# Performance work log

Measured on AMD Instinct MI355X. Metric: run time of the kernel, lower is better.

Reference implementation:

```python
import jax, jax.numpy as jnp
import numpy as np

B, S, D = 8, 8192, 64
N_HASHES = 8
BUCKET_SIZE = 64
N_BUCKETS = S // BUCKET_SIZE  # 128
SELF_ATTN_VALUE = -5e4  # torch reformer TOKEN_SELF_ATTN_VALUE


def setup_inputs() -> dict:
    key = jax.random.key(0)
    k1, k2, k3 = jax.random.split(key, 3)
    qk = jax.random.normal(k1, (B, S, D), dtype=jnp.float32)
    v = jax.random.normal(k2, (B, S, D), dtype=jnp.float32)
    # LSH random rotations: (dim, n_hashes, n_buckets // 2), shared across batch/heads
    rotations = jax.random.normal(k3, (D, N_HASHES, N_BUCKETS // 2), dtype=jnp.float32)
    return {"qk": qk, "v": v, "rotations": rotations, "query_len": S}


def _look_one_back(x):
    # concatenate each chunk with the preceding chunk (wrapping) along the kv axis
    x_extra = jnp.concatenate([x[:, -1:], x[:, :-1]], axis=1)
    return jnp.concatenate([x, x_extra], axis=2)


def _lsh_bucketed_dots(qk, v, rotations):
    batch, seqlen, dim = qk.shape
    n_buckets = seqlen // BUCKET_SIZE
    # --- hash vectors: rotate, concat with negation, argmax -> bucket ids ---
    rotated = jnp.einsum('btf,fhi->bhti', qk, rotations)           # (B, H, S, nb/2)
    rotated = jnp.concatenate([rotated, -rotated], axis=-1)        # (B, H, S, nb)
    buckets = jnp.argmax(rotated, axis=-1)                         # (B, H, S) int
    offsets = (jnp.arange(N_HASHES) * n_buckets)[None, :, None]    # disjoint per round
    buckets = (buckets + offsets).reshape(batch, -1)               # (B, H*S)

    # --- stable bucket sort via composite key (all keys unique) ---
    ticker = jnp.arange(N_HASHES * seqlen)[None, :]                # (1, H*S)
    buckets_and_t = seqlen * buckets + (ticker % seqlen)
    sticker = jnp.argsort(buckets_and_t, axis=-1)                  # sort permutation
    undo_sort = jnp.argsort(sticker, axis=-1)                      # inverse permutation
    st = sticker % seqlen                                          # original token ids

    # --- gather tokens into bucket order ---
    sqk = jnp.take_along_axis(qk, st[..., None], axis=1)           # (B, H*S, D)
    sv = jnp.take_along_axis(v, st[..., None], axis=1)

    n_chunks = N_HASHES * n_buckets
    bq_t = st.reshape(batch, n_chunks, BUCKET_SIZE)                # (B, C, bs)
    bqk = sqk.reshape(batch, n_chunks, BUCKET_SIZE, dim)
    bv = sv.reshape(batch, n_chunks, BUCKET_SIZE, dim)

    bq = bqk
    bk = bqk / (jnp.linalg.norm(bqk, axis=-1, keepdims=True) + 1e-6)  # unit-length keys

    bk = _look_one_back(bk)       # (B, C, 2*bs, D)
    bv = _look_one_back(bv)
    bkv_t = _look_one_back(bq_t)  # (B, C, 2*bs)

    dots = jnp.einsum('buie,buje->buij', bq, bk) * (dim ** -0.5)   # (B, C, bs, 2*bs)
    self_mask = bq_t[:, :, :, None] == bkv_t[:, :, None, :]
    dots = jnp.where(self_mask, SELF_ATTN_VALUE, dots)
    return dots, undo_sort, bv


def reference(qk, v, rotations, query_len):
    batch, seqlen, dim = qk.shape
    dots, undo_sort, bv = _lsh_bucketed_dots(qk, v, rotations)
    dots_logsumexp = jax.nn.logsumexp(dots, axis=-1, keepdims=True)
    p = jnp.exp(dots - dots_logsumexp)                             # per-bucket softmax
    bo = jnp.einsum('buij,buje->buie', p, bv)                      # (B, C, bs, D)
    so = bo.reshape(batch, -1, dim)                                # (B, H*S, D)
    slogits = dots_logsumexp.reshape(batch, -1)                    # (B, H*S)
    # undo the bucket sort
    o = jnp.take_along_axis(so, undo_sort[..., None], axis=1)
    logits = jnp.take_along_axis(slogits, undo_sort, axis=1)
    o = o.reshape(batch, N_HASHES, seqlen, dim)[:, :, :query_len]
    logits = logits.reshape(batch, N_HASHES, seqlen, 1)[:, :, :query_len]
    # combine across hash rounds, weighted by per-round logsumexp
    probs = jnp.exp(logits - jax.nn.logsumexp(logits, axis=1, keepdims=True))
    out = jnp.sum(o * probs, axis=1)                               # (B, query_len, D)
    return out
```

## Files before the change

### kernel.cpp

```cpp
#include <hip/hip_runtime.h>
#include <math.h>

#define B_  8
#define S_  8192
#define D_  64
#define H_  8
#define NB_ 128
#define NC_ 1024
#define REP_CAP 65536
#define T2_ 2e-3f

typedef _Float16 f16x8 __attribute__((ext_vector_type(8)));
typedef _Float16 f16x2 __attribute__((ext_vector_type(2)));
typedef float    f32x4 __attribute__((ext_vector_type(4)));
typedef unsigned int uint_;

#define MFMA16(A, Bv, C) __builtin_amdgcn_mfma_f32_16x16x32_f16(A, Bv, C, 0, 0, 0)

__global__ __launch_bounds__(256) void prep_rot_kernel(
    const float* __restrict__ rot, _Float16* __restrict__ rotHi,
    _Float16* __restrict__ rotLo, int* __restrict__ cnt)
{
  __shared__ float rs[64 * 64];
  const int tid = threadIdx.x, h = blockIdx.x;
  if (h == 0 && tid == 0) *cnt = 0;
#pragma unroll
  for (int it = 0; it < 16; ++it) {
    const int f = it * 4 + (tid >> 6), i = tid & 63;
    rs[f * 64 + i] = rot[f * 512 + h * 64 + i];
  }
  __syncthreads();
  const int i = tid & 63, grp = tid >> 6;
  _Float16 hi[16], lo[16];
#pragma unroll
  for (int ff = 0; ff < 16; ++ff) {
    const float x = rs[(grp * 16 + ff) * 64 + i];
    hi[ff] = (_Float16)x;
    lo[ff] = (_Float16)(x - (float)hi[ff]);
  }
  f16x8* dH = (f16x8*)(rotHi + h * 4096 + i * 64 + grp * 16);
  f16x8* dL = (f16x8*)(rotLo + h * 4096 + i * 64 + grp * 16);
  dH[0] = ((f16x8*)hi)[0]; dH[1] = ((f16x8*)hi)[1];
  dL[0] = ((f16x8*)lo)[0]; dL[1] = ((f16x8*)lo)[1];
}

__global__ __launch_bounds__(256) void prep_tok_kernel(
    const float* __restrict__ qk, const float* __restrict__ v,
    _Float16* __restrict__ q16, _Float16* __restrict__ kn16,
    _Float16* __restrict__ v16)
{
  const int gt = blockIdx.x * 64 + (threadIdx.x >> 2);
  const int qu = threadIdx.x & 3;
  const size_t off = (size_t)gt * 64 + qu * 16;
  float x[16];
#pragma unroll
  for (int k = 0; k < 4; ++k) ((float4*)x)[k] = ((const float4*)(qk + off))[k];
  float ss = 0.f;
#pragma unroll
  for (int k = 0; k < 16; ++k) ss = fmaf(x[k], x[k], ss);
  ss += __shfl_xor(ss, 1); ss += __shfl_xor(ss, 2);
  const float inv = 0.125f / (sqrtf(ss) + 1e-6f);
  f16x8 qh[2], kn[2];
#pragma unroll
  for (int j = 0; j < 16; ++j) {
    qh[j >> 3][j & 7] = (_Float16)x[j];
    kn[j >> 3][j & 7] = (_Float16)(x[j] * inv);
  }
  ((f16x8*)(q16  + off))[0] = qh[0]; ((f16x8*)(q16  + off))[1] = qh[1];
  ((f16x8*)(kn16 + off))[0] = kn[0]; ((f16x8*)(kn16 + off))[1] = kn[1];
  float y[16];
#pragma unroll
  for (int k = 0; k < 4; ++k) ((float4*)y)[k] = ((const float4*)(v + off))[k];
  f16x8 vv[2];
#pragma unroll
  for (int j = 0; j < 16; ++j) vv[j >> 3][j & 7] = (_Float16)y[j];
  ((f16x8*)(v16 + off))[0] = vv[0]; ((f16x8*)(v16 + off))[1] = vv[1];
}

__global__ __launch_bounds__(256) void hash_kernel(
    const float* __restrict__ qk,
    const _Float16* __restrict__ rotHi, const _Float16* __restrict__ rotLo,
    int* __restrict__ bucket, int* __restrict__ cnt, int2* __restrict__ list)
{
  __shared__ _Float16 rH[64 * 72];
  __shared__ _Float16 rL[64 * 72];
  const int tid  = threadIdx.x;
  const int tile = blockIdx.x & 127;
  const int b    = blockIdx.x >> 7;
  const int lane = tid & 63, w = tid >> 6;
  const int m16  = lane & 15, qd = lane >> 4;

  const int t = tile * 64 + w * 16 + m16;
  f16x8 BH0, BH1, BL0, BL1;
  {
    const float* src = qk + ((size_t)b * S_ + t) * 64 + 8 * qd;
    float x[16];
    ((float4*)x)[0] = ((const float4*)src)[0];
    ((float4*)x)[1] = ((const float4*)(src + 4))[0];
    ((float4*)x)[2] = ((const float4*)(src + 32))[0];
    ((float4*)x)[3] = ((const float4*)(src + 36))[0];
#pragma unroll
    for (int j = 0; j < 8; ++j) {
      const _Float16 h0 = (_Float16)x[j];
      BH0[j] = h0; BL0[j] = (_Float16)(x[j] - (float)h0);
      const _Float16 h1 = (_Float16)x[j + 8];
      BH1[j] = h1; BL1[j] = (_Float16)(x[j + 8] - (float)h1);
    }
  }
  const int srow = tid >> 2, scol = (tid & 3) * 16;
  const uint_ qd16 = (uint_)(qd << 4);

#pragma unroll 1
  for (int h = 0; h < 8; ++h) {
    __syncthreads();
    {
      const _Float16* sH = rotHi + h * 4096 + srow * 64 + scol;
      const _Float16* sL = rotLo + h * 4096 + srow * 64 + scol;
      *(f16x8*)(rH + srow * 72 + scol)     = ((const f16x8*)sH)[0];
      *(f16x8*)(rH + srow * 72 + scol + 8) = ((const f16x8*)sH)[1];
      *(f16x8*)(rL + srow * 72 + scol)     = ((const f16x8*)sL)[0];
      *(f16x8*)(rL + srow * 72 + scol + 8) = ((const f16x8*)sL)[1];
    }
    __syncthreads();

    f32x4 acc[4];
#pragma unroll
    for (int mt = 0; mt < 4; ++mt) acc[mt] = (f32x4){0.f, 0.f, 0.f, 0.f};
#pragma unroll
    for (int mt = 0; mt < 4; ++mt) {
      const _Float16* aH = rH + (16 * mt + m16) * 72 + 8 * qd;
      const _Float16* aL = rL + (16 * mt + m16) * 72 + 8 * qd;
      const f16x8 AH0 = *(const f16x8*)aH;
      const f16x8 AH1 = *(const f16x8*)(aH + 32);
      const f16x8 AL0 = *(const f16x8*)aL;
      const f16x8 AL1 = *(const f16x8*)(aL + 32);
      acc[mt] = MFMA16(AH0, BH0, acc[mt]);
      acc[mt] = MFMA16(AH1, BH1, acc[mt]);
      acc[mt] = MFMA16(AH0, BL0, acc[mt]);
      acc[mt] = MFMA16(AH1, BL1, acc[mt]);
      acc[mt] = MFMA16(AL0, BH0, acc[mt]);
      acc[mt] = MFMA16(AL1, BH1, acc[mt]);
    }

    float v1M = -1e30f, v2M = -1e30f, v1m = 1e30f, v2m = 1e30f;
#pragma unroll
    for (int mt = 0; mt < 4; ++mt)
#pragma unroll
      for (int rg = 0; rg < 4; ++rg) {
        uint_ u = __float_as_uint(acc[mt][rg]);
        u = (u & 0xFFFFFFC0u) | qd16 | (uint_)((mt << 2) | rg);
        const float xk = __uint_as_float(u);
        v2M = __builtin_amdgcn_fmed3f(v1M, v2M, xk);
        v1M = fmaxf(v1M, xk);
        v2m = __builtin_amdgcn_fmed3f(v1m, v2m, xk);
        v1m = fminf(v1m, xk);
      }
#pragma unroll
    for (int off = 16; off <= 32; off <<= 1) {
      const float o1M = __shfl_xor(v1M, off), o2M = __shfl_xor(v2M, off);
      v2M = __builtin_amdgcn_fmed3f(v1M, o1M, fmaxf(v2M, o2M));
      v1M = fmaxf(v1M, o1M);
      const float o1m = __shfl_xor(v1m, off), o2m = __shfl_xor(v2m, off);
      v2m = __builtin_amdgcn_fmed3f(v1m, o1m, fminf(v2m, o2m));
      v1m = fminf(v1m, o1m);
    }
    if (qd == 0) {
      const uint_ cM = __float_as_uint(v1M) & 63u;
      const uint_ cm = __float_as_uint(v1m) & 63u;
      const int ixM = 16 * (int)((cM >> 2) & 3u) + 4 * (int)(cM >> 4) + (int)(cM & 3u);
      const int ixm = 16 * (int)((cm >> 2) & 3u) + 4 * (int)(cm >> 4) + (int)(cm & 3u);
      const int bkt = (v1M >= -v1m) ? ixM : 64 + ixm;
      bucket[((size_t)(b * 8 + h)) * S_ + t] = bkt;
      const bool flag = ((v1M - v2M) < T2_) | ((v2m - v1m) < T2_) |
                        (fabsf(v1M + v1m) < T2_);
      if (flag) {
        const int s = atomicAdd(cnt, 1);
        if (s < REP_CAP) list[s] = make_int2(b * 8 + h, t);
      }
    }
  }
}

__global__ __launch_bounds__(256) void repair_kernel(
    const float* __restrict__ qk, const float* __restrict__ rot,
    const int* __restrict__ cnt, const int2* __restrict__ list,
    int* __restrict__ bucket)
{
  const int n = min(*cnt, REP_CAP);
  const int lane = threadIdx.x & 63;
  const int wid  = (blockIdx.x * 256 + threadIdx.x) >> 6;
  const int nw   = gridDim.x * 4;
  for (int idx = wid; idx < n; idx += nw) {
    const int bh = list[idx].x, t = list[idx].y;
    const int b = bh >> 3, hh = bh & 7;
    const float* qrow = qk + ((size_t)b * S_ + t) * D_;
    const float* rcol = rot + hh * 64 + lane;
    double acc = 0.0;
#pragma unroll 8
    for (int f = 0; f < 64; ++f)
      acc = fma((double)qrow[f], (double)rcol[(size_t)f * 512], acc);
    double vM = acc; int iM = lane;
    double vm = acc; int im = lane;
#pragma unroll
    for (int off = 32; off >= 1; off >>= 1) {
      const double voM = __shfl_xor(vM, off); const int ioM = __shfl_xor(iM, off);
      if (voM > vM || (voM == vM && ioM < iM)) { vM = voM; iM = ioM; }
      const double vom = __shfl_xor(vm, off); const int iom = __shfl_xor(im, off);
      if (vom < vm || (vom == vm && iom < im)) { vm = vom; im = iom; }
    }
    if (lane == 0) {
      const int bkt = (vM >= -vm) ? iM : 64 + im;
      bucket[(size_t)bh * S_ + t] = bkt;
    }
  }
}

__global__ __launch_bounds__(1024) void sort_kernel(
    const int* __restrict__ bucket, int* __restrict__ st)
{
  __shared__ uint_ hist[64 * 128];
  __shared__ unsigned short lb[S_];
  __shared__ int off[128];
  const int tid = threadIdx.x;
  const int bh  = blockIdx.x;
  const size_t base = (size_t)bh * S_;

#pragma unroll
  for (int k = 0; k < 8; ++k) hist[tid + k * 1024] = 0;
  __syncthreads();

#pragma unroll
  for (int k = 0; k < 8; ++k) {
    const int t = k * 1024 + tid;
    const int bk = bucket[base + t];
    lb[t] = (unsigned short)bk;
    const int g = t >> 6;
    atomicAdd(&hist[(g & 63) * 128 + bk], 1u << (16 * (g >> 6)));
  }
  __syncthreads();

  if (tid < 128) {
    uint_ s = 0;
#pragma unroll
    for (int g = 0; g < 64; ++g) {
      const uint_ wv = hist[g * 128 + tid];
      s += (wv & 0xFFFFu) + (wv >> 16);
    }
    off[tid] = (int)s;
  }
  __syncthreads();
  if (tid == 0) {
    int run = 0;
    for (int k = 0; k < 128; ++k) { const int c = off[k]; off[k] = run; run += c; }
  }
  __syncthreads();
  if (tid < 128) {
    uint_ run = (uint_)off[tid];
#pragma unroll
    for (int g = 0; g < 64; ++g) {
      const uint_ wv = hist[g * 128 + tid];
      hist[g * 128 + tid] = (wv & 0xFFFF0000u) | run;
      run += (wv & 0xFFFFu);
    }
#pragma unroll
    for (int g = 0; g < 64; ++g) {
      const uint_ wv = hist[g * 128 + tid];
      hist[g * 128 + tid] = (wv & 0xFFFFu) | (run << 16);
      run += (wv >> 16);
    }
  }
  __syncthreads();

  const int lane = tid & 63, wv_ = tid >> 6;
  const int b = bh >> 3, h = bh & 7;
  const size_t stb = (size_t)b * (H_ * S_) + (size_t)h * S_;
  const unsigned long long ltmask = (1ull << lane) - 1ull;
#pragma unroll
  for (int k = 0; k < 8; ++k) {
    const int g = wv_ * 8 + k;
    const int t = g * 64 + lane;
    const int bk = (int)lb[t];
    unsigned long long same = ~0ull;
#pragma unroll
    for (int bit = 0; bit < 7; ++bit) {
      const unsigned long long m = __ballot((bk >> bit) & 1);
      same &= ((bk >> bit) & 1) ? m : ~m;
    }
    const int rloc = __popcll(same & ltmask);
    const uint_ wd = hist[(g & 63) * 128 + bk];
    const int gbase = (int)((wd >> (16 * (g >> 6))) & 0xFFFFu);
    st[stb + gbase + rloc] = t;
  }
}

__global__ __launch_bounds__(256, 8) void attn_kernel(
    const _Float16* __restrict__ q16, const _Float16* __restrict__ kn16,
    const _Float16* __restrict__ v16, const int* __restrict__ st,
    _Float16* __restrict__ so, float* __restrict__ slog)
{
  __shared__ _Float16 smem[64 * 136];
  __shared__ __align__(16) int sIds[128];

  const int tid = threadIdx.x;
  const int c   = blockIdx.x & (NC_ - 1);
  const int b   = blockIdx.x >> 10;
  const int cm1 = (c + NC_ - 1) & (NC_ - 1);
  const size_t bst = (size_t)b * (H_ * S_);
  const size_t row0 = bst + (size_t)c * 64;
  const size_t row1 = bst + (size_t)cm1 * 64;

  const int lane = tid & 63;
  const int w    = tid >> 6;
  const int m16  = lane & 15;
  const int qd   = lane >> 4;

  if (tid < 128) sIds[tid] = (tid < 64) ? st[row0 + tid] : st[row1 + tid - 64];

  const int rid = st[row0 + 16 * w + m16];
  f16x8 q0, q1;
  {
    const _Float16* qp = q16 + ((size_t)b * S_ + rid) * 64 + 8 * qd;
    q0 = *(const f16x8*)qp;
    q1 = *(const f16x8*)(qp + 32);
  }

  const int r = tid >> 2, qu = tid & 3;
  {
    const int tok = st[row0 + r];
    const f16x8* sk = (const f16x8*)(kn16 + ((size_t)b * S_ + tok) * 64 + qu * 16);
    *(f16x8*)(smem + r * 72 + qu * 16)     = sk[0];
    *(f16x8*)(smem + r * 72 + qu * 16 + 8) = sk[1];
  }
  __syncthreads();

  f32x4 acc[8];
#pragma unroll
  for (int jt = 0; jt < 8; ++jt) acc[jt] = (f32x4){0.f, 0.f, 0.f, 0.f};

#pragma unroll
  for (int jt = 0; jt < 4; ++jt) {
    const _Float16* krow = smem + (16 * jt + m16) * 72;
    const f16x8 kb0 = *(const f16x8*)(krow + 8 * qd);
    const f16x8 kb1 = *(const f16x8*)(krow + 32 + 8 * qd);
    acc[jt] = MFMA16(kb0, q0, acc[jt]);
    acc[jt] = MFMA16(kb1, q1, acc[jt]);
  }
  __syncthreads();

  {
    const int tok = sIds[64 + r];
    const f16x8* sk = (const f16x8*)(kn16 + ((size_t)b * S_ + tok) * 64 + qu * 16);
    *(f16x8*)(smem + r * 72 + qu * 16)     = sk[0];
    *(f16x8*)(smem + r * 72 + qu * 16 + 8) = sk[1];
  }
  __syncthreads();

#pragma unroll
  for (int jt = 4; jt < 8; ++jt) {
    const _Float16* krow = smem + (16 * (jt - 4) + m16) * 72;
    const f16x8 kb0 = *(const f16x8*)(krow + 8 * qd);
    const f16x8 kb1 = *(const f16x8*)(krow + 32 + 8 * qd);
    acc[jt] = MFMA16(kb0, q0, acc[jt]);
    acc[jt] = MFMA16(kb1, q1, acc[jt]);
  }

  float m = -1e30f;
#pragma unroll
  for (int jt = 0; jt < 8; ++jt) {
    const int4 cid = *(const int4*)(sIds + 16 * jt + 4 * qd);
    float x;
    x = acc[jt][0]; if (cid.x == rid) x = -5e4f; acc[jt][0] = x; m = fmaxf(m, x);
    x = acc[jt][1]; if (cid.y == rid) x = -5e4f; acc[jt][1] = x; m = fmaxf(m, x);
    x = acc[jt][2]; if (cid.z == rid) x = -5e4f; acc[jt][2] = x; m = fmaxf(m, x);
    x = acc[jt][3]; if (cid.w == rid) x = -5e4f; acc[jt][3] = x; m = fmaxf(m, x);
  }
  m = fmaxf(m, __shfl_xor(m, 16));
  m = fmaxf(m, __shfl_xor(m, 32));
  float sum = 0.f;
#pragma unroll
  for (int jt = 0; jt < 8; ++jt)
#pragma unroll
    for (int rg = 0; rg < 4; ++rg) {
      const float e = __expf(acc[jt][rg] - m);
      acc[jt][rg] = e;
      sum += e;
    }
  sum += __shfl_xor(sum, 16);
  sum += __shfl_xor(sum, 32);
  const float rinv = 1.f / sum;

  const int hh = c >> 7;
  const size_t hb = ((size_t)(b * 8 + hh)) * S_;
  if (qd == 0) slog[hb + rid] = m + __logf(sum);

  f16x8 pa[4];
#pragma unroll
  for (int s = 0; s < 4; ++s)
#pragma unroll
    for (int j = 0; j < 8; ++j)
      pa[s][j] = (_Float16)acc[2 * s + (j >> 2)][j & 3];

  const int jp = r;
  const int c0 = 2 * jp;
  const int k0 = 32 * (c0 >> 5) + 16 * ((c0 >> 2) & 1) + 4 * ((c0 >> 3) & 3) + (c0 & 3);
  const int tok0 = sIds[k0], tok1 = sIds[k0 + 1];
  f16x8 va[2], vb[2];
  {
    const f16x8* s0 = (const f16x8*)(v16 + ((size_t)b * S_ + tok0) * 64 + qu * 16);
    const f16x8* s1 = (const f16x8*)(v16 + ((size_t)b * S_ + tok1) * 64 + qu * 16);
    va[0] = s0[0]; va[1] = s0[1];
    vb[0] = s1[0]; vb[1] = s1[1];
  }
  __syncthreads();

  {
    const int swz = (qu << 3) ^ ((qu & 1) << 5);
    _Float16* dst = smem + (c0 ^ swz);
#pragma unroll
    for (int jj = 0; jj < 16; ++jj) {
      const int d = 16 * qu + jj;
      f16x2 pk; pk[0] = va[jj >> 3][jj & 7]; pk[1] = vb[jj >> 3][jj & 7];
      *(f16x2*)(dst + d * 136) = pk;
    }
  }
  __syncthreads();

  f32x4 oacc[4];
#pragma unroll
  for (int dt = 0; dt < 4; ++dt) oacc[dt] = (f32x4){0.f, 0.f, 0.f, 0.f};
#pragma unroll
  for (int s = 0; s < 4; ++s) {
#pragma unroll
    for (int dt = 0; dt < 4; ++dt) {
      const _Float16* vp = smem + (16 * dt + m16) * 136
                         + 32 * (s ^ (dt & 1)) + 8 * (qd ^ dt);
      const f16x8 bv = *(const f16x8*)vp;
      oacc[dt] = MFMA16(pa[s], bv, oacc[dt]);
    }
  }

  const int4 rid4 = *(const int4*)(sIds + 16 * w + 4 * qd);
  const int ridv[4] = {rid4.x, rid4.y, rid4.z, rid4.w};
  float rin[4];
#pragma unroll
  for (int rg = 0; rg < 4; ++rg) rin[rg] = __shfl(rinv, 4 * qd + rg);
#pragma unroll
  for (int dt = 0; dt < 4; ++dt)
#pragma unroll
    for (int rg = 0; rg < 4; ++rg)
      so[(hb + ridv[rg]) * 64 + 16 * dt + m16] = (_Float16)(oacc[dt][rg] * rin[rg]);
}

__global__ __launch_bounds__(256) void combine_kernel(
    const _Float16* __restrict__ so, const float* __restrict__ slog,
    float* __restrict__ out)
{
  const int gt = blockIdx.x * 4 + (threadIdx.x >> 6);
  const int d  = threadIdx.x & 63;
  const int b  = gt >> 13;
  const int t  = gt & (S_ - 1);

  float l[8];
#pragma unroll
  for (int h = 0; h < 8; ++h)
    l[h] = slog[((size_t)(b * 8 + h)) * S_ + t];
  float m = l[0];
#pragma unroll
  for (int h = 1; h < 8; ++h) m = fmaxf(m, l[h]);
  float wv[8], W = 0.f;
#pragma unroll
  for (int h = 0; h < 8; ++h) { wv[h] = expf(l[h] - m); W += wv[h]; }
  const float iW = 1.f / W;
  float acc = 0.f;
#pragma unroll
  for (int h = 0; h < 8; ++h)
    acc = fmaf(wv[h], (float)so[(((size_t)(b * 8 + h)) * S_ + t) * 64 + d], acc);
  out[(size_t)gt * 64 + d] = acc * iW;
}

extern "C" void kernel_launch(void* const* d_in, const int* in_sizes, int n_in,
                              void* d_out, int out_size, void* d_ws, size_t ws_size,
                              hipStream_t stream)
{
  const float* qk  = (const float*)d_in[0];
  const float* v   = (const float*)d_in[1];
  const float* rot = (const float*)d_in[2];
  float* out = (float*)d_out;

  char* ws = (char*)d_ws;
  const size_t MB = 1ull << 20, KB = 1024;
  int*      bucket = (int*)      (ws + 0 * MB);
  int*      st     = (int*)      (ws + 2 * MB);
  float*    slog   = (float*)    (ws + 4 * MB);
  _Float16* q16    = (_Float16*) (ws + 8 * MB);
  _Float16* kn16   = (_Float16*) (ws + 16 * MB);
  _Float16* v16    = (_Float16*) (ws + 24 * MB);
  _Float16* rotHi  = (_Float16*) (ws + 32 * MB);
  _Float16* rotLo  = (_Float16*) (ws + 32 * MB + 64 * KB);
  int*      cnt    = (int*)      (ws + 32 * MB + 128 * KB);
  int2*     list   = (int2*)     (ws + 32 * MB + 192 * KB);
  _Float16* so     = (_Float16*) (ws + 33 * MB);
  if (ws_size < 98 * MB) return;

  hipLaunchKernelGGL(prep_rot_kernel, dim3(8),           dim3(256),  0, stream, rot, rotHi, rotLo, cnt);
  hipLaunchKernelGGL(prep_tok_kernel, dim3(1024),        dim3(256),  0, stream, qk, v, q16, kn16, v16);
  hipLaunchKernelGGL(hash_kernel,     dim3(8 * 128),     dim3(256),  0, stream, qk, rotHi, rotLo, bucket, cnt, list);
  hipLaunchKernelGGL(repair_kernel,   dim3(128),         dim3(256),  0, stream, qk, rot, cnt, list, bucket);
  hipLaunchKernelGGL(sort_kernel,     dim3(64),          dim3(1024), 0, stream, bucket, st);
  hipLaunchKernelGGL(attn_kernel,     dim3(B_ * NC_),    dim3(256),  0, stream, q16, kn16, v16, st, so, slog);
  hipLaunchKernelGGL(combine_kernel,  dim3(B_ * S_ / 4), dim3(256),  0, stream, so, slog, out);
}
```

Baseline: 195.0 us.

## Merge prep kernels, stage attention output through LDS, vectorize combine

Folds the rotation-prep and token-prep kernels into one launch, with the first 8 blocks handling the rotations. The attention kernel now writes its normalized output tile to shared memory and then stores each token row as 16-byte vectors, replacing scattered 2-byte global stores. The combine kernel gives each thread 8 output dims and uses vectorized f16x8 loads and float4 stores. Together these aim to cut launch overhead and uncoalesced memory traffic, at the cost of extra barriers in the attention kernel.

```diff
diff --git a/kernel.cpp b/kernel.cpp
--- a/kernel.cpp
+++ b/kernel.cpp
@@ -17,40 +17,42 @@
 
 #define MFMA16(A, Bv, C) __builtin_amdgcn_mfma_f32_16x16x32_f16(A, Bv, C, 0, 0, 0)
 
-__global__ __launch_bounds__(256) void prep_rot_kernel(
+__global__ __launch_bounds__(256) void prep_kernel(
     const float* __restrict__ rot, _Float16* __restrict__ rotHi,
-    _Float16* __restrict__ rotLo, int* __restrict__ cnt)
-{
-  __shared__ float rs[64 * 64];
-  const int tid = threadIdx.x, h = blockIdx.x;
-  if (h == 0 && tid == 0) *cnt = 0;
-#pragma unroll
-  for (int it = 0; it < 16; ++it) {
-    const int f = it * 4 + (tid >> 6), i = tid & 63;
-    rs[f * 64 + i] = rot[f * 512 + h * 64 + i];
-  }
-  __syncthreads();
-  const int i = tid & 63, grp = tid >> 6;
-  _Float16 hi[16], lo[16];
-#pragma unroll
-  for (int ff = 0; ff < 16; ++ff) {
-    const float x = rs[(grp * 16 + ff) * 64 + i];
-    hi[ff] = (_Float16)x;
-    lo[ff] = (_Float16)(x - (float)hi[ff]);
-  }
-  f16x8* dH = (f16x8*)(rotHi + h * 4096 + i * 64 + grp * 16);
-  f16x8* dL = (f16x8*)(rotLo + h * 4096 + i * 64 + grp * 16);
-  dH[0] = ((f16x8*)hi)[0]; dH[1] = ((f16x8*)hi)[1];
-  dL[0] = ((f16x8*)lo)[0]; dL[1] = ((f16x8*)lo)[1];
-}
-
-__global__ __launch_bounds__(256) void prep_tok_kernel(
+    _Float16* __restrict__ rotLo, int* __restrict__ cnt,
     const float* __restrict__ qk, const float* __restrict__ v,
     _Float16* __restrict__ q16, _Float16* __restrict__ kn16,
     _Float16* __restrict__ v16)
 {
-  const int gt = blockIdx.x * 64 + (threadIdx.x >> 2);
-  const int qu = threadIdx.x & 3;
+  __shared__ float rs[64 * 64];
+  const int tid = threadIdx.x;
+
+  if (blockIdx.x < 8) {
+    const int h = blockIdx.x;
+    if (h == 0 && tid == 0) *cnt = 0;
+#pragma unroll
+    for (int it = 0; it < 16; ++it) {
+      const int f = it * 4 + (tid >> 6), i = tid & 63;
+      rs[f * 64 + i] = rot[f * 512 + h * 64 + i];
+    }
+    __syncthreads();
+    const int i = tid & 63, grp = tid >> 6;
+    _Float16 hi[16], lo[16];
+#pragma unroll
+    for (int ff = 0; ff < 16; ++ff) {
+      const float x = rs[(grp * 16 + ff) * 64 + i];
+      hi[ff] = (_Float16)x;
+      lo[ff] = (_Float16)(x - (float)hi[ff]);
+    }
+    f16x8* dH = (f16x8*)(rotHi + h * 4096 + i * 64 + grp * 16);
+    f16x8* dL = (f16x8*)(rotLo + h * 4096 + i * 64 + grp * 16);
+    dH[0] = ((f16x8*)hi)[0]; dH[1] = ((f16x8*)hi)[1];
+    dL[0] = ((f16x8*)lo)[0]; dL[1] = ((f16x8*)lo)[1];
+    return;
+  }
+
+  const int gt = (blockIdx.x - 8) * 64 + (tid >> 2);
+  const int qu = tid & 3;
   const size_t off = (size_t)gt * 64 + qu * 16;
   float x[16];
 #pragma unroll
@@ -400,8 +402,7 @@
     for (int j = 0; j < 8; ++j)
       pa[s][j] = (_Float16)acc[2 * s + (j >> 2)][j & 3];
 
-  const int jp = r;
-  const int c0 = 2 * jp;
+  const int c0 = 2 * r;
   const int k0 = 32 * (c0 >> 5) + 16 * ((c0 >> 2) & 1) + 4 * ((c0 >> 3) & 3) + (c0 & 3);
   const int tok0 = sIds[k0], tok1 = sIds[k0 + 1];
   f16x8 va[2], vb[2];
@@ -434,36 +435,47 @@
     for (int dt = 0; dt < 4; ++dt) {
       const _Float16* vp = smem + (16 * dt + m16) * 136
                          + 32 * (s ^ (dt & 1)) + 8 * (qd ^ dt);
-      const f16x8 bv = *(const f16x8*)vp;
+      const f16x8 bv = *(const f16x8*)(vp);
       oacc[dt] = MFMA16(pa[s], bv, oacc[dt]);
     }
   }
 
-  const int4 rid4 = *(const int4*)(sIds + 16 * w + 4 * qd);
-  const int ridv[4] = {rid4.x, rid4.y, rid4.z, rid4.w};
   float rin[4];
 #pragma unroll
   for (int rg = 0; rg < 4; ++rg) rin[rg] = __shfl(rinv, 4 * qd + rg);
+
+  __syncthreads();
 #pragma unroll
   for (int dt = 0; dt < 4; ++dt)
 #pragma unroll
     for (int rg = 0; rg < 4; ++rg)
-      so[(hb + ridv[rg]) * 64 + 16 * dt + m16] = (_Float16)(oacc[dt][rg] * rin[rg]);
+      smem[(16 * w + 4 * qd + rg) * 72 + 16 * dt + m16] =
+          (_Float16)(oacc[dt][rg] * rin[rg]);
+  __syncthreads();
+
+  {
+    const int tok = sIds[r];
+    const f16x8* srcp = (const f16x8*)(smem + r * 72 + qu * 16);
+    const f16x8 o0 = srcp[0], o1 = srcp[1];
+    f16x8* dstp = (f16x8*)(so + (hb + tok) * 64 + qu * 16);
+    dstp[0] = o0; dstp[1] = o1;
+  }
 }
 
 __global__ __launch_bounds__(256) void combine_kernel(
     const _Float16* __restrict__ so, const float* __restrict__ slog,
     float* __restrict__ out)
 {
-  const int gt = blockIdx.x * 4 + (threadIdx.x >> 6);
-  const int d  = threadIdx.x & 63;
-  const int b  = gt >> 13;
-  const int t  = gt & (S_ - 1);
+  const int gid = blockIdx.x * 256 + threadIdx.x;
+  const int gt  = gid >> 3;
+  const int oct = gid & 7;
+  const int b   = gt >> 13;
+  const int t   = gt & (S_ - 1);
+  const size_t base8 = (size_t)(b * 8) * S_ + t;
 
   float l[8];
 #pragma unroll
-  for (int h = 0; h < 8; ++h)
-    l[h] = slog[((size_t)(b * 8 + h)) * S_ + t];
+  for (int h = 0; h < 8; ++h) l[h] = slog[base8 + (size_t)h * S_];
   float m = l[0];
 #pragma unroll
   for (int h = 1; h < 8; ++h) m = fmaxf(m, l[h]);
@@ -471,11 +483,19 @@
 #pragma unroll
   for (int h = 0; h < 8; ++h) { wv[h] = expf(l[h] - m); W += wv[h]; }
   const float iW = 1.f / W;
-  float acc = 0.f;
-#pragma unroll
-  for (int h = 0; h < 8; ++h)
-    acc = fmaf(wv[h], (float)so[(((size_t)(b * 8 + h)) * S_ + t) * 64 + d], acc);
-  out[(size_t)gt * 64 + d] = acc * iW;
+
+  float acc[8] = {0.f, 0.f, 0.f, 0.f, 0.f, 0.f, 0.f, 0.f};
+#pragma unroll
+  for (int h = 0; h < 8; ++h) {
+    const f16x8 vv = *(const f16x8*)(so + (base8 + (size_t)h * S_) * 64 + oct * 8);
+#pragma unroll
+    for (int j = 0; j < 8; ++j) acc[j] = fmaf(wv[h], (float)vv[j], acc[j]);
+  }
+  float4 o0, o1;
+  o0.x = acc[0] * iW; o0.y = acc[1] * iW; o0.z = acc[2] * iW; o0.w = acc[3] * iW;
+  o1.x = acc[4] * iW; o1.y = acc[5] * iW; o1.z = acc[6] * iW; o1.w = acc[7] * iW;
+  float4* dst = (float4*)(out + (size_t)gt * 64 + oct * 8);
+  dst[0] = o0; dst[1] = o1;
 }
 
 extern "C" void kernel_launch(void* const* d_in, const int* in_sizes, int n_in,
@@ -502,11 +522,16 @@
   _Float16* so     = (_Float16*) (ws + 33 * MB);
   if (ws_size < 98 * MB) return;
 
-  hipLaunchKernelGGL(prep_rot_kernel, dim3(8),           dim3(256),  0, stream, rot, rotHi, rotLo, cnt);
-  hipLaunchKernelGGL(prep_tok_kernel, dim3(1024),        dim3(256),  0, stream, qk, v, q16, kn16, v16);
-  hipLaunchKernelGGL(hash_kernel,     dim3(8 * 128),     dim3(256),  0, stream, qk, rotHi, rotLo, bucket, cnt, list);
-  hipLaunchKernelGGL(repair_kernel,   dim3(128),         dim3(256),  0, stream, qk, rot, cnt, list, bucket);
-  hipLaunchKernelGGL(sort_kernel,     dim3(64),          dim3(1024), 0, stream, bucket, st);
-  hipLaunchKernelGGL(attn_kernel,     dim3(B_ * NC_),    dim3(256),  0, stream, q16, kn16, v16, st, so, slog);
-  hipLaunchKernelGGL(combine_kernel,  dim3(B_ * S_ / 4), dim3(256),  0, stream, so, slog, out);
-}
+  hipLaunchKernelGGL(prep_kernel,    dim3(8 + 1024),      dim3(256),  0, stream,
+                     rot, rotHi, rotLo, cnt, qk, v, q16, kn16, v16);
+  hipLaunchKernelGGL(hash_kernel,    dim3(8 * 128),       dim3(256),  0, stream,
+                     qk, rotHi, rotLo, bucket, cnt, list);
+  hipLaunchKernelGGL(repair_kernel,  dim3(128),           dim3(256),  0, stream,
+                     qk, rot, cnt, list, bucket);
+  hipLaunchKernelGGL(sort_kernel,    dim3(64),            dim3(1024), 0, stream,
+                     bucket, st);
+  hipLaunchKernelGGL(attn_kernel,    dim3(B_ * NC_),      dim3(256),  0, stream,
+                     q16, kn16, v16, st, so, slog);
+  hipLaunchKernelGGL(combine_kernel, dim3(B_ * S_ * 8 / 256), dim3(256), 0, stream,
+                     so, slog, out);
+}
```

After: 191.2 us. No clear change (-1.9%).
